# Performance work log

Measured on AMD Instinct MI355X. Metric: run time of the kernel, lower is better.

## Reference

```python
import jax, jax.numpy as jnp
import numpy as np

B, S, D, H, L, F = 16, 256, 512, 1024, 2, 2048  # batch, seq, inner, head(clusters), layers, ffnn
HID = D // 2
LN_EPS = 1e-5


def _lstm_dir(x, Wih, Whh, bih, bhh, reverse=False):
    # x: [B,S,D] -> hs: [B,S,HID]; PyTorch gate order i,f,g,o
    if reverse:
        x = x[:, ::-1]
    xT = jnp.swapaxes(x, 0, 1)                    # [S,B,D]
    pre = xT @ Wih.T + (bih + bhh)                # precompute input contribution [S,B,4*HID]
    z = jnp.zeros((x.shape[0], Whh.shape[1]), x.dtype)

    def step(carry, p):
        h, c = carry
        g = p + h @ Whh.T
        i, f, gg, o = jnp.split(g, 4, axis=-1)
        c = jax.nn.sigmoid(f) * c + jax.nn.sigmoid(i) * jnp.tanh(gg)
        h = jax.nn.sigmoid(o) * jnp.tanh(c)
        return (h, c), h

    _, hs = jax.lax.scan(step, (z, z), pre)
    hs = jnp.swapaxes(hs, 0, 1)                   # [B,S,HID]
    if reverse:
        hs = hs[:, ::-1]
    return hs


def _layernorm(x, g, b):
    mu = jnp.mean(x, axis=-1, keepdims=True)
    var = jnp.mean(jnp.square(x - mu), axis=-1, keepdims=True)
    return (x - mu) * jax.lax.rsqrt(var + LN_EPS) * g + b


def _forward(input_sequence, label_embeddings, out_proj,
             Wih_f, Whh_f, bih_f, bhh_f, Wih_b, Whh_b, bih_b, bhh_b,
             ffnn_w1, ffnn_b1, ffnn_w2, ffnn_b2, ln_g, ln_b):
    fwd = _lstm_dir(input_sequence, Wih_f, Whh_f, bih_f, bhh_f, reverse=False)
    bwd = _lstm_dir(input_sequence, Wih_b, Whh_b, bih_b, bhh_b, reverse=True)
    features = jnp.concatenate([fwd, bwd], axis=-1)          # [B,S,D]

    query = jnp.broadcast_to(label_embeddings, (input_sequence.shape[0], H, D))
    for l in range(L):
        # self-attention (no scaling, as in source)
        w = jax.nn.softmax(jnp.einsum('bqd,bkd->bqk', query, query), axis=-1)
        q1 = jnp.einsum('bqk,bkd->bqd', w, query)
        # cross-attention onto LSTM features
        w2 = jax.nn.softmax(jnp.einsum('bqd,bsd->bqs', q1, features), axis=-1)
        q2 = jnp.einsum('bqs,bsd->bqd', w2, features)
        # FFN + LayerNorm
        h = jax.nn.gelu(q2 @ ffnn_w1[l] + ffnn_b1[l], approximate=False) @ ffnn_w2[l] + ffnn_b2[l]
        query = _layernorm(h, ln_g[l], ln_b[l])
    # (query @ output) * eye @ ones  ==  diagonal of the matmul == batched dot
    return jnp.einsum('bhd,dh->bh', query, out_proj)


def setup_inputs() -> dict:
    ks = jax.random.split(jax.random.key(0), 20)
    s_lstm = 1.0 / np.sqrt(HID)
    s_ff = 0.02
    clusters = jax.random.normal(ks[0], (H, D), jnp.float32) * s_ff
    return {
        'input_sequence': jax.random.normal(ks[1], (B, S, D), jnp.float32),
        'label_embeddings': clusters,
        'out_proj': clusters.T,
        'Wih_f': jax.random.normal(ks[2], (4 * HID, D), jnp.float32) * s_lstm,
        'Whh_f': jax.random.normal(ks[3], (4 * HID, HID), jnp.float32) * s_lstm,
        'bih_f': jax.random.normal(ks[4], (4 * HID,), jnp.float32) * s_lstm,
        'bhh_f': jax.random.normal(ks[5], (4 * HID,), jnp.float32) * s_lstm,
        'Wih_b': jax.random.normal(ks[6], (4 * HID, D), jnp.float32) * s_lstm,
        'Whh_b': jax.random.normal(ks[7], (4 * HID, HID), jnp.float32) * s_lstm,
        'bih_b': jax.random.normal(ks[8], (4 * HID,), jnp.float32) * s_lstm,
        'bhh_b': jax.random.normal(ks[9], (4 * HID,), jnp.float32) * s_lstm,
        'ffnn_w1': jax.random.normal(ks[10], (L, D, F), jnp.float32) * s_ff,
        'ffnn_b1': jnp.zeros((L, F), jnp.float32),
        'ffnn_w2': jax.random.normal(ks[11], (L, F, D), jnp.float32) * s_ff,
        'ffnn_b2': jnp.zeros((L, D), jnp.float32),
        'ln_g': jnp.ones((L, D), jnp.float32),
        'ln_b': jnp.zeros((L, D), jnp.float32),
    }


def reference(input_sequence, label_embeddings, out_proj,
              Wih_f, Whh_f, bih_f, bhh_f, Wih_b, Whh_b, bih_b, bhh_b,
              ffnn_w1, ffnn_b1, ffnn_w2, ffnn_b2, ln_g, ln_b):
    return _forward(input_sequence, label_embeddings, out_proj,
                    Wih_f, Whh_f, bih_f, bhh_f, Wih_b, Whh_b, bih_b, bhh_b,
                    ffnn_w1, ffnn_b1, ffnn_w2, ffnn_b2, ln_g, ln_b)
```

## Files before the change

kernel.cpp:

```cpp
#include <hip/hip_runtime.h>
#include <hip/hip_bf16.h>
#include <math.h>

#define NB 16
#define NS 256
#define ND 512
#define NH 1024
#define NF 2048
#define NHID 256

typedef __attribute__((ext_vector_type(8))) short bf16x8;
typedef __attribute__((ext_vector_type(4))) float f32x4;

__device__ __forceinline__ unsigned short f2bf(float f) {
    unsigned u = __float_as_uint(f);
    unsigned r = u + 0x7fffu + ((u >> 16) & 1u);
    return (unsigned short)(r >> 16);
}
__device__ __forceinline__ float bf2f(unsigned short h) {
    return __uint_as_float(((unsigned)h) << 16);
}
__device__ __forceinline__ float sigmoid_fast(float x) {
    return 1.0f / (1.0f + __expf(-x));
}
__device__ __forceinline__ float tanh_fast(float x) {
    return 1.0f - 2.0f / (__expf(2.0f * x) + 1.0f);
}

template<int PASSES, int ACT, int OUT>
__global__ __launch_bounds__(256) void sgemm4(
    const unsigned short* __restrict__ Ahi, const unsigned short* __restrict__ Alo,
    const unsigned short* __restrict__ Bhi, const unsigned short* __restrict__ Blo,
    const float* __restrict__ bias,
    float* __restrict__ C, unsigned short* __restrict__ Chi, unsigned short* __restrict__ Clo,
    int M, int N, int K, int lda, int ldb, long sA, long sB, long sC)
{
    __shared__ unsigned short Ah[128 * 32];
    __shared__ unsigned short Bh[128 * 32];
    __shared__ unsigned short Al[(PASSES == 3) ? 128 * 32 : 64];
    __shared__ unsigned short Bl[(PASSES == 3) ? 128 * 32 : 64];

    const int t = threadIdx.x;
    const int z = blockIdx.z;
    const int m0 = blockIdx.y * 128, n0 = blockIdx.x * 128;
    const int wid = t >> 6, lane = t & 63;
    const int wr = (wid >> 1) * 64, wc = (wid & 1) * 64;
    const int lr = lane & 15, lk = lane >> 4;
    const int rl = lane >> 2, sl = lane & 3;

    const unsigned short* pAh = Ahi + (size_t)z * sA;
    const unsigned short* pBh = Bhi + (size_t)z * sB;
    const unsigned short* pAl = (PASSES == 3) ? Alo + (size_t)z * sA : nullptr;
    const unsigned short* pBl = (PASSES == 3) ? Blo + (size_t)z * sB : nullptr;

    f32x4 acc[4][4];
    #pragma unroll
    for (int i = 0; i < 4; ++i)
        #pragma unroll
        for (int j = 0; j < 4; ++j) acc[i][j] = (f32x4){0.f, 0.f, 0.f, 0.f};

    for (int k0 = 0; k0 < K; k0 += 32) {
        #pragma unroll
        for (int e = 0; e < 2; ++e) {
            const int r = e * 64 + wid * 16 + rl;
            const size_t goA = (size_t)(m0 + r) * lda + k0 + sl * 8;
            const size_t goB = (size_t)(n0 + r) * ldb + k0 + sl * 8;
            const int lo = (e * 64 + wid * 16) * 32;
            __builtin_amdgcn_global_load_lds((const void*)(pAh + goA), (void*)&Ah[lo], 16, 0, 0);
            __builtin_amdgcn_global_load_lds((const void*)(pBh + goB), (void*)&Bh[lo], 16, 0, 0);
            if (PASSES == 3) {
                __builtin_amdgcn_global_load_lds((const void*)(pAl + goA), (void*)&Al[lo], 16, 0, 0);
                __builtin_amdgcn_global_load_lds((const void*)(pBl + goB), (void*)&Bl[lo], 16, 0, 0);
            }
        }
        __syncthreads();

        bf16x8 ah[4], bh[4], al[4], bl[4];
        #pragma unroll
        for (int mt = 0; mt < 4; ++mt) {
            int rf = wr + mt * 16 + lr;
            ah[mt] = *(const bf16x8*)&Ah[rf * 32 + lk * 8];
            if (PASSES == 3) al[mt] = *(const bf16x8*)&Al[rf * 32 + lk * 8];
        }
        #pragma unroll
        for (int nt = 0; nt < 4; ++nt) {
            int rf = wc + nt * 16 + lr;
            bh[nt] = *(const bf16x8*)&Bh[rf * 32 + lk * 8];
            if (PASSES == 3) bl[nt] = *(const bf16x8*)&Bl[rf * 32 + lk * 8];
        }
        #pragma unroll
        for (int mt = 0; mt < 4; ++mt)
            #pragma unroll
            for (int nt = 0; nt < 4; ++nt) {
                acc[mt][nt] = __builtin_amdgcn_mfma_f32_16x16x32_bf16(ah[mt], bh[nt], acc[mt][nt], 0, 0, 0);
                if (PASSES == 3) {
                    acc[mt][nt] = __builtin_amdgcn_mfma_f32_16x16x32_bf16(al[mt], bh[nt], acc[mt][nt], 0, 0, 0);
                    acc[mt][nt] = __builtin_amdgcn_mfma_f32_16x16x32_bf16(ah[mt], bl[nt], acc[mt][nt], 0, 0, 0);
                }
            }
        __syncthreads();
    }

    #pragma unroll
    for (int nt = 0; nt < 4; ++nt) {
        int col = n0 + wc + nt * 16 + lr;
        float bv = bias ? bias[col] : 0.0f;
        #pragma unroll
        for (int mt = 0; mt < 4; ++mt) {
            #pragma unroll
            for (int i = 0; i < 4; ++i) {
                int row = m0 + wr + mt * 16 + lk * 4 + i;
                float x = acc[mt][nt][i] + bv;
                if (ACT == 1) x = 0.5f * x * (1.0f + erff(x * 0.70710678118654752f));
                size_t oi = (size_t)z * sC + (size_t)row * N + col;
                if (OUT == 1) {
                    unsigned short h = f2bf(x);
                    Chi[oi] = h;
                    Clo[oi] = f2bf(x - bf2f(h));
                } else if (OUT == 2) {
                    Chi[oi] = f2bf(x);
                } else {
                    C[oi] = x;
                }
            }
        }
    }
}

static void gemm4(int passes, int act, int outm,
                  const unsigned short* Ahi, const unsigned short* Alo,
                  const unsigned short* Bhi, const unsigned short* Blo,
                  const float* bias, float* C, unsigned short* Chi, unsigned short* Clo,
                  int M, int N, int K, int lda, int ldb,
                  long sA, long sB, long sC, int Z, hipStream_t st)
{
    dim3 g(N / 128, M / 128, Z), b(256);
    if (passes == 3) {
        sgemm4<3, 0, 0><<<g, b, 0, st>>>(Ahi, Alo, Bhi, Blo, bias, C, Chi, Clo, M, N, K, lda, ldb, sA, sB, sC);
    } else if (outm == 1) {
        sgemm4<1, 0, 1><<<g, b, 0, st>>>(Ahi, Alo, Bhi, Blo, bias, C, Chi, Clo, M, N, K, lda, ldb, sA, sB, sC);
    } else if (outm == 2 && act == 1) {
        sgemm4<1, 1, 2><<<g, b, 0, st>>>(Ahi, Alo, Bhi, Blo, bias, C, Chi, Clo, M, N, K, lda, ldb, sA, sB, sC);
    } else if (outm == 2) {
        sgemm4<1, 0, 2><<<g, b, 0, st>>>(Ahi, Alo, Bhi, Blo, bias, C, Chi, Clo, M, N, K, lda, ldb, sA, sB, sC);
    } else {
        sgemm4<1, 0, 0><<<g, b, 0, st>>>(Ahi, Alo, Bhi, Blo, bias, C, Chi, Clo, M, N, K, lda, ldb, sA, sB, sC);
    }
}

__global__ __launch_bounds__(256) void cvt_split(const float* __restrict__ in,
                                                 unsigned short* __restrict__ hi,
                                                 unsigned short* __restrict__ lo)
{
    size_t i = ((size_t)blockIdx.x * 256 + threadIdx.x) * 4;
    float4 v = *(const float4*)(in + i);
    ushort4 h, l;
    h.x = f2bf(v.x); l.x = f2bf(v.x - bf2f(h.x));
    h.y = f2bf(v.y); l.y = f2bf(v.y - bf2f(h.y));
    h.z = f2bf(v.z); l.z = f2bf(v.z - bf2f(h.z));
    h.w = f2bf(v.w); l.w = f2bf(v.w - bf2f(h.w));
    *(ushort4*)(hi + i) = h;
    *(ushort4*)(lo + i) = l;
}

__global__ __launch_bounds__(256) void cvt_split_t(const float* __restrict__ in,
                                                   unsigned short* __restrict__ hiT,
                                                   unsigned short* __restrict__ loT,
                                                   int R, int C)
{
    __shared__ unsigned short tileH[64 * 72];
    __shared__ unsigned short tileL[64 * 72];
    int r0 = blockIdx.y * 64, c0 = blockIdx.x * 64;
    int t = threadIdx.x;
    int tr = t >> 2, tc = (t & 3) * 16;

    float v[16];
    const float* src = in + (size_t)(r0 + tr) * C + c0 + tc;
    *(float4*)(v)      = *(const float4*)(src);
    *(float4*)(v + 4)  = *(const float4*)(src + 4);
    *(float4*)(v + 8)  = *(const float4*)(src + 8);
    *(float4*)(v + 12) = *(const float4*)(src + 12);
    #pragma unroll
    for (int i = 0; i < 16; ++i) {
        unsigned short h = f2bf(v[i]);
        tileH[(tc + i) * 72 + tr] = h;
        tileL[(tc + i) * 72 + tr] = f2bf(v[i] - bf2f(h));
    }
    __syncthreads();

    size_t ob = (size_t)(c0 + tr) * R + r0 + tc;
    *(uint4*)(hiT + ob)     = *(const uint4*)(&tileH[tr * 72 + tc]);
    *(uint4*)(hiT + ob + 8) = *(const uint4*)(&tileH[tr * 72 + tc + 8]);
    *(uint4*)(loT + ob)     = *(const uint4*)(&tileL[tr * 72 + tc]);
    *(uint4*)(loT + ob + 8) = *(const uint4*)(&tileL[tr * 72 + tc + 8]);
}

__global__ __launch_bounds__(256) void tcvt_bf16(const unsigned short* __restrict__ in,
                                                 unsigned short* __restrict__ out,
                                                 int R, int C)
{
    __shared__ unsigned short tile[64 * 72];
    int z = blockIdx.z;
    in += (size_t)z * R * C;
    out += (size_t)z * R * C;
    int r0 = blockIdx.y * 64, c0 = blockIdx.x * 64;
    int t = threadIdx.x;
    int tr = t >> 2, tc = (t & 3) * 16;

    uint4 q0 = *(const uint4*)(in + (size_t)(r0 + tr) * C + c0 + tc);
    uint4 q1 = *(const uint4*)(in + (size_t)(r0 + tr) * C + c0 + tc + 8);
    unsigned short e[16];
    *(uint4*)(e) = q0;
    *(uint4*)(e + 8) = q1;
    #pragma unroll
    for (int i = 0; i < 16; ++i) tile[(tc + i) * 72 + tr] = e[i];
    __syncthreads();

    uint4 o0 = *(const uint4*)(&tile[tr * 72 + tc]);
    uint4 o1 = *(const uint4*)(&tile[tr * 72 + tc + 8]);
    *(uint4*)(out + (size_t)(c0 + tr) * R + r0 + tc) = o0;
    *(uint4*)(out + (size_t)(c0 + tr) * R + r0 + tc + 8) = o1;
}

__global__ __launch_bounds__(256) void bias_sum_kernel(
    const float* bihF, const float* bhhF, const float* bihB, const float* bhhB,
    float* out)
{
    int i = blockIdx.x * 256 + threadIdx.x;
    if (i < 1024) out[i] = bihF[i] + bhhF[i];
    else out[i] = bihB[i - 1024] + bhhB[i - 1024];
}

__global__ __launch_bounds__(256) void rec_fused(
    const float* __restrict__ pre,
    const float* __restrict__ WhhF, const float* __restrict__ WhhB,
    unsigned long long* __restrict__ hg, int* __restrict__ flags,
    unsigned short* __restrict__ fhi, unsigned short* __restrict__ flo,
    const unsigned short* __restrict__ lehi, const unsigned short* __restrict__ lelo,
    float* __restrict__ wsc,
    const float* __restrict__ w1, const float* __restrict__ w2,
    unsigned short* __restrict__ w1th0, unsigned short* __restrict__ w2th0,
    unsigned short* __restrict__ w1th1, unsigned short* __restrict__ w2th1,
    const float* __restrict__ proj,
    unsigned short* __restrict__ pth, unsigned short* __restrict__ ptl)
{
    __shared__ unsigned short hh[16 * 264];
    __shared__ unsigned short hl[16 * 264];
    __shared__ float gx[4][16][17];
    __shared__ unsigned short gAh[128 * 32];
    __shared__ unsigned short gAl[128 * 32];
    __shared__ unsigned short gBh[128 * 32];
    __shared__ unsigned short gBl[128 * 32];
    __shared__ unsigned short tH[64 * 72];
    __shared__ unsigned short tL[64 * 72];

    const int tid = threadIdx.x;

    if (blockIdx.x < 32) {
        const int bid = blockIdx.x;
        const int dir = bid >> 4, slice = bid & 15;
        const float* Whh = dir ? WhhB : WhhF;
        const int wv = tid >> 6;
        const int lane = tid & 63;
        const int lr = lane & 15;
        const int lk = lane >> 4;
        const int eb = tid >> 4;
        const int eu = tid & 15;

        bf16x8 wfh[8], wfl[8];
        {
            const float* wrow = Whh + (size_t)(wv * 256 + slice * 16 + lr) * 256 + lk * 8;
            #pragma unroll
            for (int kt = 0; kt < 8; ++kt) {
                float4 a = *(const float4*)(wrow + kt * 32);
                float4 b = *(const float4*)(wrow + kt * 32 + 4);
                float v[8] = {a.x, a.y, a.z, a.w, b.x, b.y, b.z, b.w};
                unsigned short hhv[8], llv[8];
                #pragma unroll
                for (int i = 0; i < 8; ++i) {
                    unsigned short h = f2bf(v[i]);
                    hhv[i] = h;
                    llv[i] = f2bf(v[i] - bf2f(h));
                }
                wfh[kt] = *(bf16x8*)hhv;
                wfl[kt] = *(bf16x8*)llv;
            }
        }
        for (int i = tid; i < 16 * 264; i += 256) { hh[i] = 0; hl[i] = 0; }

        float c = 0.0f;
        __syncthreads();

        for (int si = 0; si < NS; ++si) {
            const int s = dir ? (NS - 1 - si) : si;
            const float* pp = pre + ((size_t)(eb * NS + s)) * 2048 + dir * 1024 + slice * 16 + eu;
            float pi = pp[0], pf = pp[256], pg = pp[512], po = pp[768];

            if (si > 0) {
                if (tid < 16) {
                    while (__hip_atomic_load(&flags[dir * 16 + tid], __ATOMIC_RELAXED,
                                             __HIP_MEMORY_SCOPE_AGENT) < si) {
                        __builtin_amdgcn_s_sleep(1);
                    }
                }
                __syncthreads();
                const unsigned long long* src =
                    hg + (size_t)(((si - 1) & 1) * 2 + dir) * 2048;
                const int b2 = tid >> 4, pb = (tid & 15) * 8;
                unsigned short hbuf[16], lbuf[16];
                #pragma unroll
                for (int j = 0; j < 8; ++j) {
                    unsigned long long v = __hip_atomic_load(
                        &src[b2 * 128 + pb + j], __ATOMIC_RELAXED,
                        __HIP_MEMORY_SCOPE_AGENT);
                    hbuf[2 * j]     = (unsigned short)(v & 0xffff);
                    lbuf[2 * j]     = (unsigned short)((v >> 16) & 0xffff);
                    hbuf[2 * j + 1] = (unsigned short)((v >> 32) & 0xffff);
                    lbuf[2 * j + 1] = (unsigned short)(v >> 48);
                }
                char* dh = (char*)hh + b2 * 528 + (tid & 15) * 32;
                char* dl = (char*)hl + b2 * 528 + (tid & 15) * 32;
                *(uint4*)dh        = *(uint4*)(hbuf);
                *(uint4*)(dh + 16) = *(uint4*)(hbuf + 8);
                *(uint4*)dl        = *(uint4*)(lbuf);
                *(uint4*)(dl + 16) = *(uint4*)(lbuf + 8);
                __syncthreads();
            }

            f32x4 acc = (f32x4){0.f, 0.f, 0.f, 0.f};
            #pragma unroll
            for (int kt = 0; kt < 8; ++kt) {
                const char* hp = (const char*)hh + lr * 528 + kt * 64 + lk * 16;
                const char* lp = (const char*)hl + lr * 528 + kt * 64 + lk * 16;
                bf16x8 ah = *(const bf16x8*)hp;
                bf16x8 al = *(const bf16x8*)lp;
                acc = __builtin_amdgcn_mfma_f32_16x16x32_bf16(ah, wfh[kt], acc, 0, 0, 0);
                acc = __builtin_amdgcn_mfma_f32_16x16x32_bf16(al, wfh[kt], acc, 0, 0, 0);
                acc = __builtin_amdgcn_mfma_f32_16x16x32_bf16(ah, wfl[kt], acc, 0, 0, 0);
            }
            #pragma unroll
            for (int i = 0; i < 4; ++i) gx[wv][lk * 4 + i][lr] = acc[i];
            __syncthreads();

            float ai = gx[0][eb][eu] + pi;
            float af = gx[1][eb][eu] + pf;
            float ag = gx[2][eb][eu] + pg;
            float ao = gx[3][eb][eu] + po;
            float gi = sigmoid_fast(ai);
            float gf = sigmoid_fast(af);
            float gg = tanh_fast(ag);
            float go = sigmoid_fast(ao);
            c = gf * c + gi * gg;
            float h = go * tanh_fast(c);

            unsigned short h16 = f2bf(h);
            unsigned short l16 = f2bf(h - bf2f(h16));
            unsigned my = (unsigned)h16 | ((unsigned)l16 << 16);
            unsigned oth = __shfl_xor(my, 1);
            if ((eu & 1) == 0) {
                unsigned long long v = (unsigned long long)my |
                                       ((unsigned long long)oth << 32);
                unsigned long long* dst =
                    hg + (size_t)((si & 1) * 2 + dir) * 2048;
                __hip_atomic_store(&dst[eb * 128 + slice * 8 + (eu >> 1)], v,
                                   __ATOMIC_RELAXED, __HIP_MEMORY_SCOPE_AGENT);
            }
            size_t oi = ((size_t)(eb * NS + s)) * 512 + dir * 256 + slice * 16 + eu;
            fhi[oi] = h16;
            flo[oi] = l16;

            asm volatile("s_waitcnt vmcnt(0)" ::: "memory");
            __syncthreads();
            if (tid == 0)
                __hip_atomic_store(&flags[bid], si + 1, __ATOMIC_RELAXED,
                                   __HIP_MEMORY_SCOPE_AGENT);
        }
        return;
    }

    const int hid = blockIdx.x - 32;
    const int lane = tid & 63;
    const int wid = tid >> 6;
    const int lr = lane & 15, lk = lane >> 4;

    if (hid < 64) {
        const int m0 = (hid >> 3) * 128, n0 = (hid & 7) * 128;
        const int wr = (wid >> 1) * 64, wc = (wid & 1) * 64;
        const int sr = tid >> 1, sc = (tid & 1) * 16;

        f32x4 acc[4][4];
        #pragma unroll
        for (int i = 0; i < 4; ++i)
            #pragma unroll
            for (int j = 0; j < 4; ++j) acc[i][j] = (f32x4){0.f, 0.f, 0.f, 0.f};

        for (int k0 = 0; k0 < ND; k0 += 32) {
            {
                size_t oa = (size_t)(m0 + sr) * ND + k0 + sc;
                size_t ob = (size_t)(n0 + sr) * ND + k0 + sc;
                *(uint4*)&gAh[sr * 32 + sc]     = *(const uint4*)(lehi + oa);
                *(uint4*)&gAh[sr * 32 + sc + 8] = *(const uint4*)(lehi + oa + 8);
                *(uint4*)&gAl[sr * 32 + sc]     = *(const uint4*)(lelo + oa);
                *(uint4*)&gAl[sr * 32 + sc + 8] = *(const uint4*)(lelo + oa + 8);
                *(uint4*)&gBh[sr * 32 + sc]     = *(const uint4*)(lehi + ob);
                *(uint4*)&gBh[sr * 32 + sc + 8] = *(const uint4*)(lehi + ob + 8);
                *(uint4*)&gBl[sr * 32 + sc]     = *(const uint4*)(lelo + ob);
                *(uint4*)&gBl[sr * 32 + sc + 8] = *(const uint4*)(lelo + ob + 8);
            }
            __syncthreads();

            bf16x8 ah[4], al[4], bh[4], bl[4];
            #pragma unroll
            for (int mt = 0; mt < 4; ++mt) {
                int rf = wr + mt * 16 + lr;
                ah[mt] = *(const bf16x8*)&gAh[rf * 32 + lk * 8];
                al[mt] = *(const bf16x8*)&gAl[rf * 32 + lk * 8];
            }
            #pragma unroll
            for (int nt = 0; nt < 4; ++nt) {
                int rf = wc + nt * 16 + lr;
                bh[nt] = *(const bf16x8*)&gBh[rf * 32 + lk * 8];
                bl[nt] = *(const bf16x8*)&gBl[rf * 32 + lk * 8];
            }
            #pragma unroll
            for (int mt = 0; mt < 4; ++mt)
                #pragma unroll
                for (int nt = 0; nt < 4; ++nt) {
                    acc[mt][nt] = __builtin_amdgcn_mfma_f32_16x16x32_bf16(ah[mt], bh[nt], acc[mt][nt], 0, 0, 0);
                    acc[mt][nt] = __builtin_amdgcn_mfma_f32_16x16x32_bf16(al[mt], bh[nt], acc[mt][nt], 0, 0, 0);
                    acc[mt][nt] = __builtin_amdgcn_mfma_f32_16x16x32_bf16(ah[mt], bl[nt], acc[mt][nt], 0, 0, 0);
                }
            __syncthreads();
        }
        const int wr2 = (wid >> 1) * 64, wc2 = (wid & 1) * 64;
        #pragma unroll
        for (int nt = 0; nt < 4; ++nt) {
            int col = n0 + wc2 + nt * 16 + lr;
            #pragma unroll
            for (int mt = 0; mt < 4; ++mt)
                #pragma unroll
                for (int i = 0; i < 4; ++i) {
                    int row = m0 + wr2 + mt * 16 + lk * 4 + i;
                    wsc[(size_t)row * NH + col] = acc[mt][nt][i];
                }
        }
    }

    const int tr = tid >> 2, tc = (tid & 3) * 16;
    for (int job = hid; job < 1152; job += 224) {
        const float* in;
        unsigned short* outH;
        unsigned short* outL = nullptr;
        int R, C, by, bx;
        if (job < 256)        { int j = job;        in = w1;              outH = w1th0; R = ND; C = NF; by = j >> 5, bx = j & 31; }
        else if (job < 512)   { int j = job - 256;  in = w2;              outH = w2th0; R = NF; C = ND; by = j >> 3, bx = j & 7; }
        else if (job < 768)   { int j = job - 512;  in = w1 + (size_t)ND * NF; outH = w1th1; R = ND; C = NF; by = j >> 5, bx = j & 31; }
        else if (job < 1024)  { int j = job - 768;  in = w2 + (size_t)NF * ND; outH = w2th1; R = NF; C = ND; by = j >> 3, bx = j & 7; }
        else                  { int j = job - 1024; in = proj;            outH = pth; outL = ptl; R = 512; C = 1024; by = j >> 4, bx = j & 15; }

        int r0 = by * 64, c0 = bx * 64;
        __syncthreads();
        float v[16];
        const float* src = in + (size_t)(r0 + tr) * C + c0 + tc;
        *(float4*)(v)      = *(const float4*)(src);
        *(float4*)(v + 4)  = *(const float4*)(src + 4);
        *(float4*)(v + 8)  = *(const float4*)(src + 8);
        *(float4*)(v + 12) = *(const float4*)(src + 12);
        if (outL) {
            #pragma unroll
            for (int i = 0; i < 16; ++i) {
                unsigned short h = f2bf(v[i]);
                tH[(tc + i) * 72 + tr] = h;
                tL[(tc + i) * 72 + tr] = f2bf(v[i] - bf2f(h));
            }
        } else {
            #pragma unroll
            for (int i = 0; i < 16; ++i) tH[(tc + i) * 72 + tr] = f2bf(v[i]);
        }
        __syncthreads();
        size_t ob = (size_t)(c0 + tr) * R + r0 + tc;
        *(uint4*)(outH + ob)     = *(const uint4*)(&tH[tr * 72 + tc]);
        *(uint4*)(outH + ob + 8) = *(const uint4*)(&tH[tr * 72 + tc + 8]);
        if (outL) {
            *(uint4*)(outL + ob)     = *(const uint4*)(&tL[tr * 72 + tc]);
            *(uint4*)(outL + ob + 8) = *(const uint4*)(&tL[tr * 72 + tc + 8]);
        }
    }
}

__global__ __launch_bounds__(256) void softmax_ip(float* __restrict__ X, int N)
{
    float* row = X + (size_t)blockIdx.x * N;
    unsigned short* o = (unsigned short*)row;
    int t = threadIdx.x;
    int cnt = N >> 8;
    float v[4];
    float m = -1e30f;
    for (int i = 0; i < cnt; ++i) { v[i] = row[t + (i << 8)]; m = fmaxf(m, v[i]); }
    for (int sh = 32; sh; sh >>= 1) m = fmaxf(m, __shfl_xor(m, sh));
    __shared__ float lm[4];
    if ((t & 63) == 0) lm[t >> 6] = m;
    __syncthreads();
    m = fmaxf(fmaxf(lm[0], lm[1]), fmaxf(lm[2], lm[3]));
    float s = 0.0f;
    for (int i = 0; i < cnt; ++i) { v[i] = expf(v[i] - m); s += v[i]; }
    for (int sh = 32; sh; sh >>= 1) s += __shfl_xor(s, sh);
    __shared__ float ls[4];
    if ((t & 63) == 0) ls[t >> 6] = s;
    __syncthreads();
    s = ls[0] + ls[1] + ls[2] + ls[3];
    float inv = 1.0f / s;
    __syncthreads();
    for (int i = 0; i < cnt; ++i) {
        float y = v[i] * inv;
        unsigned short h = f2bf(y);
        int j = t + (i << 8);
        o[j] = h;
        o[N + j] = f2bf(y - bf2f(h));
    }
}

__global__ __launch_bounds__(256) void layernorm_split(
    const float* __restrict__ X, const float* __restrict__ g, const float* __restrict__ b,
    unsigned short* __restrict__ ohi, unsigned short* __restrict__ olo)
{
    const float* row = X + (size_t)blockIdx.x * 512;
    size_t ob = (size_t)blockIdx.x * 512;
    int t = threadIdx.x;
    float x0 = row[t], x1 = row[t + 256];
    float s = x0 + x1, sq = x0 * x0 + x1 * x1;
    for (int o = 32; o; o >>= 1) { s += __shfl_xor(s, o); sq += __shfl_xor(sq, o); }
    __shared__ float ls[8];
    int w = t >> 6;
    if ((t & 63) == 0) { ls[w] = s; ls[4 + w] = sq; }
    __syncthreads();
    s = ls[0] + ls[1] + ls[2] + ls[3];
    sq = ls[4] + ls[5] + ls[6] + ls[7];
    float mu = s * (1.0f / 512.0f);
    float var = sq * (1.0f / 512.0f) - mu * mu;
    float inv = rsqrtf(var + 1e-5f);
    float y0 = (x0 - mu) * inv * g[t]       + b[t];
    float y1 = (x1 - mu) * inv * g[t + 256] + b[t + 256];
    unsigned short h0 = f2bf(y0), h1 = f2bf(y1);
    ohi[ob + t]       = h0;  olo[ob + t]       = f2bf(y0 - bf2f(h0));
    ohi[ob + t + 256] = h1;  olo[ob + t + 256] = f2bf(y1 - bf2f(h1));
}

__global__ __launch_bounds__(256) void outproj3(
    const unsigned short* __restrict__ qhi, const unsigned short* __restrict__ qlo,
    const unsigned short* __restrict__ phi, const unsigned short* __restrict__ plo,
    float* __restrict__ out)
{
    int gw = blockIdx.x * 4 + (threadIdx.x >> 6);
    int lane = threadIdx.x & 63;
    int h = gw & 1023;
    uint4 qh = ((const uint4*)(qhi + (size_t)gw * 512))[lane];
    uint4 ql = ((const uint4*)(qlo + (size_t)gw * 512))[lane];
    uint4 ph = ((const uint4*)(phi + (size_t)h * 512))[lane];
    uint4 pl = ((const uint4*)(plo + (size_t)h * 512))[lane];
    unsigned short qhe[8], qle[8], phe[8], ple[8];
    *(uint4*)qhe = qh; *(uint4*)qle = ql; *(uint4*)phe = ph; *(uint4*)ple = pl;
    float s = 0.0f;
    #pragma unroll
    for (int i = 0; i < 8; ++i) {
        float q = bf2f(qhe[i]) + bf2f(qle[i]);
        float p = bf2f(phe[i]) + bf2f(ple[i]);
        s += q * p;
    }
    for (int o = 32; o; o >>= 1) s += __shfl_xor(s, o);
    if (lane == 0) out[gw] = s;
}

extern "C" void kernel_launch(void* const* d_in, const int* in_sizes, int n_in,
                              void* d_out, int out_size, void* d_ws, size_t ws_size,
                              hipStream_t stream)
{
    (void)in_sizes; (void)n_in; (void)out_size; (void)ws_size;

    const float* x     = (const float*)d_in[0];
    const float* le    = (const float*)d_in[1];
    const float* proj  = (const float*)d_in[2];
    const float* WihF  = (const float*)d_in[3];
    const float* WhhF  = (const float*)d_in[4];
    const float* bihF  = (const float*)d_in[5];
    const float* bhhF  = (const float*)d_in[6];
    const float* WihB  = (const float*)d_in[7];
    const float* WhhB  = (const float*)d_in[8];
    const float* bihB  = (const float*)d_in[9];
    const float* bhhB  = (const float*)d_in[10];
    const float* w1    = (const float*)d_in[11];
    const float* b1    = (const float*)d_in[12];
    const float* w2    = (const float*)d_in[13];
    const float* b2    = (const float*)d_in[14];
    const float* lng   = (const float*)d_in[15];
    const float* lnb   = (const float*)d_in[16];
    float* out = (float*)d_out;
    float* ws  = (float*)d_ws;
    unsigned short* wsu = (unsigned short*)d_ws;

    const size_t MEG = 1048576;
    const size_t R0    = 0;
    const size_t R1    = 8 * MEG;
    const size_t AR    = 16 * MEG;
    const size_t QHI   = 33 * MEG;
    const size_t QLO   = 37 * MEG;
    const size_t FHI   = 41 * MEG;
    const size_t FLO   = 42 * MEG;
    const size_t FTHI  = 43 * MEG;
    const size_t FTLO  = 44 * MEG;
    const size_t LEHI  = 45 * MEG;
    const size_t LELO  = LEHI  + MEG / 4;
    const size_t LETHI = LELO  + MEG / 4;
    const size_t LETLO = LETHI + MEG / 4;
    const size_t WIHH  = 46 * MEG;
    const size_t WIHL  = WIHH + MEG / 2;
    const size_t SYNC  = 47 * MEG;
    const size_t W1TH0 = SYNC  + MEG / 4;
    const size_t W1TH1 = W1TH0 + MEG / 2;
    const size_t W2TH0 = W1TH1 + MEG / 2;
    const size_t W2TH1 = W2TH0 + MEG / 2;
    const size_t PTH   = W2TH1 + MEG / 2;
    const size_t PTL   = PTH   + MEG / 4;
    const size_t BSUM  = PTL   + MEG / 4;

    float* pre    = ws + R0;
    float* lnsrc  = ws + R0;
    float* arena  = ws + AR;
    float* bsum   = ws + BSUM;
    int*   flags  = (int*)(ws + SYNC);
    unsigned long long* hg = (unsigned long long*)(ws + SYNC + 1024);
    unsigned short* qthi  = wsu + 2 * R0;
    unsigned short* q2hi  = wsu + 2 * R1;
    unsigned short* qhi   = wsu + 2 * QHI;
    unsigned short* qlo   = wsu + 2 * QLO;
    unsigned short* fhi   = wsu + 2 * FHI;
    unsigned short* flo   = wsu + 2 * FLO;
    unsigned short* fthi  = wsu + 2 * FTHI;
    unsigned short* ftlo  = wsu + 2 * FTLO;
    unsigned short* lehi  = wsu + 2 * LEHI;
    unsigned short* lelo  = wsu + 2 * LELO;
    unsigned short* lethi = wsu + 2 * LETHI;
    unsigned short* letlo = wsu + 2 * LETLO;
    unsigned short* wihh  = wsu + 2 * WIHH;
    unsigned short* wihl  = wsu + 2 * WIHL;
    unsigned short* w1th0 = wsu + 2 * W1TH0;
    unsigned short* w1th1 = wsu + 2 * W1TH1;
    unsigned short* w2th0 = wsu + 2 * W2TH0;
    unsigned short* w2th1 = wsu + 2 * W2TH1;
    unsigned short* pth   = wsu + 2 * PTH;
    unsigned short* ptl   = wsu + 2 * PTL;

    bias_sum_kernel<<<8, 256, 0, stream>>>(bihF, bhhF, bihB, bhhB, bsum);
    cvt_split<<<512, 256, 0, stream>>>(WihF, wihh, wihl);
    cvt_split<<<512, 256, 0, stream>>>(WihB, wihh + 524288, wihl + 524288);
    cvt_split<<<512, 256, 0, stream>>>(le, lehi, lelo);
    { dim3 g(512 / 64, 1024 / 64, 1);
      cvt_split_t<<<g, 256, 0, stream>>>(le, lethi, letlo, 1024, 512); }
    hipMemsetAsync(flags, 0, 32 * sizeof(int), stream);

    unsigned short* xhi = wsu + 2 * AR;
    unsigned short* xlo = wsu + 2 * (AR + MEG);
    cvt_split<<<2048, 256, 0, stream>>>(x, xhi, xlo);

    gemm4(3, 0, 0, xhi, xlo, wihh, wihl, bsum, pre, nullptr, nullptr,
          NB * NS, 2048, ND, ND, ND, 0, 0, 0, 1, stream);

    float* wsc_l0 = arena;
    rec_fused<<<256, 256, 0, stream>>>(pre, WhhF, WhhB, hg, flags, fhi, flo,
                                       lehi, lelo, wsc_l0,
                                       w1, w2, w1th0, w2th0, w1th1, w2th1,
                                       proj, pth, ptl);
    { dim3 g(512 / 64, 256 / 64, 16);
      tcvt_bf16<<<g, 256, 0, stream>>>(fhi, fthi, 256, 512);
      tcvt_bf16<<<g, 256, 0, stream>>>(flo, ftlo, 256, 512); }

    for (int l = 0; l < 2; ++l) {
        const float* b1l = b1 + (size_t)l * NF;
        const float* b2l = b2 + (size_t)l * ND;
        const float* gl  = lng + (size_t)l * ND;
        const float* bl  = lnb + (size_t)l * ND;
        unsigned short* w1th = l ? w1th1 : w1th0;
        unsigned short* w2th = l ? w2th1 : w2th0;

        if (l == 0) {
            float* wsc = wsc_l0;
            unsigned short* wscu = (unsigned short*)wsc;
            unsigned short* q1hi = wsu + 2 * (AR + 1 * MEG);
            unsigned short* q1lo = wsu + 2 * (AR + 1 * MEG + MEG / 4);
            float* s2s = arena + 4 * MEG;
            unsigned short* s2u = (unsigned short*)s2s;

            softmax_ip<<<NH, 256, 0, stream>>>(wsc, NH);
            gemm4(1, 0, 1, wscu, nullptr, lethi, nullptr, nullptr, nullptr, q1hi, q1lo,
                  NH, ND, NH, 2 * NH, NH, 0, 0, 0, 1, stream);
            gemm4(3, 0, 0, q1hi, q1lo, fhi, flo, nullptr, s2s, nullptr, nullptr,
                  NH, NS, ND, ND, ND, 0, (long)NS * ND, (long)NH * NS, 16, stream);
            softmax_ip<<<NB * NH, 256, 0, stream>>>(s2s, NS);
            gemm4(1, 0, 2, s2u, nullptr, fthi, nullptr, nullptr, nullptr, q2hi, nullptr,
                  NH, ND, NS, 2 * NS, NS,
                  (long)2 * NH * NS, (long)ND * NS, (long)NH * ND, 16, stream);
        } else {
            { dim3 g(512 / 64, 1024 / 64, 16);
              tcvt_bf16<<<g, 256, 0, stream>>>(qhi, qthi, 1024, 512); }
            float* wsc = arena;
            unsigned short* wscu = (unsigned short*)wsc;
            unsigned short* q1hi = wsu + 2 * (AR + 8 * MEG);
            unsigned short* q1lo = wsu + 2 * (AR + 10 * MEG);
            float* s2s = arena + 12 * MEG;
            unsigned short* s2u = (unsigned short*)s2s;
            for (int g8 = 0; g8 < 2; ++g8) {
                size_t qo = (size_t)g8 * 8;
                gemm4(3, 0, 0, qhi + qo * NH * ND, qlo + qo * NH * ND,
                      qhi + qo * NH * ND, qlo + qo * NH * ND, nullptr, wsc, nullptr, nullptr,
                      NH, NH, ND, ND, ND,
                      (long)NH * ND, (long)NH * ND, (long)NH * NH, 8, stream);
                softmax_ip<<<8 * NH, 256, 0, stream>>>(wsc, NH);
                gemm4(1, 0, 1, wscu, nullptr, qthi + qo * ND * NH, nullptr,
                      nullptr, nullptr, q1hi, q1lo, NH, ND, NH, 2 * NH, NH,
                      (long)2 * NH * NH, (long)ND * NH, (long)NH * ND, 8, stream);
                gemm4(3, 0, 0, q1hi, q1lo, fhi + qo * NS * ND, flo + qo * NS * ND,
                      nullptr, s2s, nullptr, nullptr, NH, NS, ND, ND, ND,
                      (long)NH * ND, (long)NS * ND, (long)NH * NS, 8, stream);
                softmax_ip<<<8 * NH, 256, 0, stream>>>(s2s, NS);
                gemm4(1, 0, 2, s2u, nullptr, fthi + qo * ND * NS, nullptr,
                      nullptr, nullptr, q2hi + qo * NH * ND, nullptr,
                      NH, ND, NS, 2 * NS, NS,
                      (long)2 * NH * NS, (long)ND * NS, (long)NH * ND, 8, stream);
            }
        }

        unsigned short* ffhi = wsu + 2 * AR;
        gemm4(1, 1, 2, q2hi, nullptr, w1th, nullptr, b1l, nullptr, ffhi, nullptr,
              16384, NF, ND, ND, ND, 0, 0, 0, 1, stream);
        gemm4(1, 0, 0, ffhi, nullptr, w2th, nullptr, b2l, lnsrc, nullptr, nullptr,
              16384, ND, NF, NF, NF, 0, 0, 0, 1, stream);
        layernorm_split<<<NB * NH, 256, 0, stream>>>(lnsrc, gl, bl, qhi, qlo);
    }

    outproj3<<<4096, 256, 0, stream>>>(qhi, qlo, pth, ptl, out);
}
```

Before: 1.510 ms.

## Fuse FFN second GEMM with LayerNorm and merge post-recurrence transposes with softmax

Adds an ffn2_ln kernel in which each block computes a 64x512 full-row output tile of the second FFN GEMM, then applies bias and LayerNorm in registers and writes the bf16 hi/lo split directly. This removes the fp32 intermediate round trip and the separate layernorm launch. It also merges the two feature transposes and the layer-0 self-attention softmax into one post_rec launch. The cost is that the fused GEMM launches only 256 blocks with a simple single-buffered K loop, which may use the GPU less efficiently than the tuned 128x128 GEMM.

New measurement: 1.502 ms. About the same (-0.5%).

```diff
diff --git a/kernel.cpp b/kernel.cpp
--- a/kernel.cpp
+++ b/kernel.cpp
@@ -146,6 +146,124 @@
     } else {
         sgemm4<1, 0, 0><<<g, b, 0, st>>>(Ahi, Alo, Bhi, Blo, bias, C, Chi, Clo, M, N, K, lda, ldb, sA, sB, sC);
     }
+}
+
+__global__ __launch_bounds__(256) void ffn2_ln(
+    const unsigned short* __restrict__ A, const unsigned short* __restrict__ B,
+    const float* __restrict__ bias, const float* __restrict__ g, const float* __restrict__ bb,
+    unsigned short* __restrict__ Ohi, unsigned short* __restrict__ Olo)
+{
+    __shared__ unsigned short Ah[64 * 32];
+    __shared__ unsigned short Bh[512 * 32];
+    __shared__ float stats[64][4][2];
+
+    const int t = threadIdx.x;
+    const int m0 = blockIdx.x * 64;
+    const int wid = t >> 6, lane = t & 63;
+    const int lr = lane & 15, lk = lane >> 4;
+    const int wc = wid * 128;
+    const int rl = lane >> 2, sl = lane & 3;
+
+    f32x4 acc[4][8];
+    #pragma unroll
+    for (int i = 0; i < 4; ++i)
+        #pragma unroll
+        for (int j = 0; j < 8; ++j) acc[i][j] = (f32x4){0.f, 0.f, 0.f, 0.f};
+
+    for (int k0 = 0; k0 < NF; k0 += 32) {
+        __builtin_amdgcn_global_load_lds(
+            (const void*)(A + (size_t)(m0 + wid * 16 + rl) * NF + k0 + sl * 8),
+            (void*)&Ah[(wid * 16) * 32], 16, 0, 0);
+        #pragma unroll
+        for (int e = 0; e < 8; ++e) {
+            int r = e * 64 + wid * 16 + rl;
+            __builtin_amdgcn_global_load_lds(
+                (const void*)(B + (size_t)r * NF + k0 + sl * 8),
+                (void*)&Bh[(e * 64 + wid * 16) * 32], 16, 0, 0);
+        }
+        __syncthreads();
+
+        bf16x8 af[4], bf[8];
+        #pragma unroll
+        for (int mt = 0; mt < 4; ++mt)
+            af[mt] = *(const bf16x8*)&Ah[(mt * 16 + lr) * 32 + lk * 8];
+        #pragma unroll
+        for (int nt = 0; nt < 8; ++nt)
+            bf[nt] = *(const bf16x8*)&Bh[(wc + nt * 16 + lr) * 32 + lk * 8];
+        #pragma unroll
+        for (int mt = 0; mt < 4; ++mt)
+            #pragma unroll
+            for (int nt = 0; nt < 8; ++nt)
+                acc[mt][nt] = __builtin_amdgcn_mfma_f32_16x16x32_bf16(af[mt], bf[nt], acc[mt][nt], 0, 0, 0);
+        __syncthreads();
+    }
+
+    float bv[8];
+    #pragma unroll
+    for (int nt = 0; nt < 8; ++nt) bv[nt] = bias[wc + nt * 16 + lr];
+
+    float psum[4][4], psq[4][4];
+    #pragma unroll
+    for (int mt = 0; mt < 4; ++mt)
+        #pragma unroll
+        for (int i = 0; i < 4; ++i) {
+            float s = 0.f, q = 0.f;
+            #pragma unroll
+            for (int nt = 0; nt < 8; ++nt) {
+                float x = acc[mt][nt][i] + bv[nt];
+                acc[mt][nt][i] = x;
+                s += x;
+                q += x * x;
+            }
+            psum[mt][i] = s;
+            psq[mt][i] = q;
+        }
+    #pragma unroll
+    for (int o = 1; o <= 8; o <<= 1)
+        #pragma unroll
+        for (int mt = 0; mt < 4; ++mt)
+            #pragma unroll
+            for (int i = 0; i < 4; ++i) {
+                psum[mt][i] += __shfl_xor(psum[mt][i], o);
+                psq[mt][i]  += __shfl_xor(psq[mt][i], o);
+            }
+    if (lr == 0) {
+        #pragma unroll
+        for (int mt = 0; mt < 4; ++mt)
+            #pragma unroll
+            for (int i = 0; i < 4; ++i) {
+                int r = mt * 16 + lk * 4 + i;
+                stats[r][wid][0] = psum[mt][i];
+                stats[r][wid][1] = psq[mt][i];
+            }
+    }
+    __syncthreads();
+
+    float gv[8], betav[8];
+    #pragma unroll
+    for (int nt = 0; nt < 8; ++nt) {
+        gv[nt]    = g[wc + nt * 16 + lr];
+        betav[nt] = bb[wc + nt * 16 + lr];
+    }
+    #pragma unroll
+    for (int mt = 0; mt < 4; ++mt)
+        #pragma unroll
+        for (int i = 0; i < 4; ++i) {
+            int r = mt * 16 + lk * 4 + i;
+            float s = stats[r][0][0] + stats[r][1][0] + stats[r][2][0] + stats[r][3][0];
+            float q = stats[r][0][1] + stats[r][1][1] + stats[r][2][1] + stats[r][3][1];
+            float mu = s * (1.0f / 512.0f);
+            float var = q * (1.0f / 512.0f) - mu * mu;
+            float inv = rsqrtf(var + 1e-5f);
+            #pragma unroll
+            for (int nt = 0; nt < 8; ++nt) {
+                float y = (acc[mt][nt][i] - mu) * inv * gv[nt] + betav[nt];
+                size_t oi = (size_t)(m0 + r) * 512 + wc + nt * 16 + lr;
+                unsigned short h = f2bf(y);
+                Ohi[oi] = h;
+                Olo[oi] = f2bf(y - bf2f(h));
+            }
+        }
 }
 
 __global__ __launch_bounds__(256) void cvt_split(const float* __restrict__ in,
@@ -488,6 +606,73 @@
     }
 }
 
+__global__ __launch_bounds__(256) void post_rec(
+    const unsigned short* __restrict__ fhi, const unsigned short* __restrict__ flo,
+    unsigned short* __restrict__ fthi, unsigned short* __restrict__ ftlo,
+    float* __restrict__ wsc)
+{
+    __shared__ unsigned short tile[64 * 72];
+    __shared__ float lm[4];
+    __shared__ float ls[4];
+    const int t = threadIdx.x;
+
+    if (blockIdx.x < 1024) {
+        int job = blockIdx.x;
+        const unsigned short* in;
+        unsigned short* out;
+        if (job < 512) { in = fhi; out = fthi; } else { in = flo; out = ftlo; job -= 512; }
+        const int R = 256, C = 512;
+        int z = job >> 5, jj = job & 31;
+        int bx = jj & 7, by = jj >> 3;
+        in  += (size_t)z * R * C;
+        out += (size_t)z * R * C;
+        int r0 = by * 64, c0 = bx * 64;
+        int tr = t >> 2, tc = (t & 3) * 16;
+
+        uint4 q0 = *(const uint4*)(in + (size_t)(r0 + tr) * C + c0 + tc);
+        uint4 q1 = *(const uint4*)(in + (size_t)(r0 + tr) * C + c0 + tc + 8);
+        unsigned short e[16];
+        *(uint4*)(e) = q0;
+        *(uint4*)(e + 8) = q1;
+        #pragma unroll
+        for (int i = 0; i < 16; ++i) tile[(tc + i) * 72 + tr] = e[i];
+        __syncthreads();
+
+        *(uint4*)(out + (size_t)(c0 + tr) * R + r0 + tc)     = *(const uint4*)(&tile[tr * 72 + tc]);
+        *(uint4*)(out + (size_t)(c0 + tr) * R + r0 + tc + 8) = *(const uint4*)(&tile[tr * 72 + tc + 8]);
+        return;
+    }
+
+    const int N = 1024;
+    float* row = wsc + (size_t)(blockIdx.x - 1024) * N;
+    unsigned short* o = (unsigned short*)row;
+    float v[4];
+    float m = -1e30f;
+    #pragma unroll
+    for (int i = 0; i < 4; ++i) { v[i] = row[t + (i << 8)]; m = fmaxf(m, v[i]); }
+    for (int sh = 32; sh; sh >>= 1) m = fmaxf(m, __shfl_xor(m, sh));
+    if ((t & 63) == 0) lm[t >> 6] = m;
+    __syncthreads();
+    m = fmaxf(fmaxf(lm[0], lm[1]), fmaxf(lm[2], lm[3]));
+    float s = 0.0f;
+    #pragma unroll
+    for (int i = 0; i < 4; ++i) { v[i] = expf(v[i] - m); s += v[i]; }
+    for (int sh = 32; sh; sh >>= 1) s += __shfl_xor(s, sh);
+    if ((t & 63) == 0) ls[t >> 6] = s;
+    __syncthreads();
+    s = ls[0] + ls[1] + ls[2] + ls[3];
+    float inv = 1.0f / s;
+    __syncthreads();
+    #pragma unroll
+    for (int i = 0; i < 4; ++i) {
+        float y = v[i] * inv;
+        unsigned short h = f2bf(y);
+        int j = t + (i << 8);
+        o[j] = h;
+        o[N + j] = f2bf(y - bf2f(h));
+    }
+}
+
 __global__ __launch_bounds__(256) void softmax_ip(float* __restrict__ X, int N)
 {
     float* row = X + (size_t)blockIdx.x * N;
@@ -520,32 +705,6 @@
     }
 }
 
-__global__ __launch_bounds__(256) void layernorm_split(
-    const float* __restrict__ X, const float* __restrict__ g, const float* __restrict__ b,
-    unsigned short* __restrict__ ohi, unsigned short* __restrict__ olo)
-{
-    const float* row = X + (size_t)blockIdx.x * 512;
-    size_t ob = (size_t)blockIdx.x * 512;
-    int t = threadIdx.x;
-    float x0 = row[t], x1 = row[t + 256];
-    float s = x0 + x1, sq = x0 * x0 + x1 * x1;
-    for (int o = 32; o; o >>= 1) { s += __shfl_xor(s, o); sq += __shfl_xor(sq, o); }
-    __shared__ float ls[8];
-    int w = t >> 6;
-    if ((t & 63) == 0) { ls[w] = s; ls[4 + w] = sq; }
-    __syncthreads();
-    s = ls[0] + ls[1] + ls[2] + ls[3];
-    sq = ls[4] + ls[5] + ls[6] + ls[7];
-    float mu = s * (1.0f / 512.0f);
-    float var = sq * (1.0f / 512.0f) - mu * mu;
-    float inv = rsqrtf(var + 1e-5f);
-    float y0 = (x0 - mu) * inv * g[t]       + b[t];
-    float y1 = (x1 - mu) * inv * g[t + 256] + b[t + 256];
-    unsigned short h0 = f2bf(y0), h1 = f2bf(y1);
-    ohi[ob + t]       = h0;  olo[ob + t]       = f2bf(y0 - bf2f(h0));
-    ohi[ob + t + 256] = h1;  olo[ob + t + 256] = f2bf(y1 - bf2f(h1));
-}
-
 __global__ __launch_bounds__(256) void outproj3(
     const unsigned short* __restrict__ qhi, const unsigned short* __restrict__ qlo,
     const unsigned short* __restrict__ phi, const unsigned short* __restrict__ plo,
@@ -624,7 +783,6 @@
     const size_t BSUM  = PTL   + MEG / 4;
 
     float* pre    = ws + R0;
-    float* lnsrc  = ws + R0;
     float* arena  = ws + AR;
     float* bsum   = ws + BSUM;
     int*   flags  = (int*)(ws + SYNC);
@@ -670,9 +828,8 @@
                                        lehi, lelo, wsc_l0,
                                        w1, w2, w1th0, w2th0, w1th1, w2th1,
                                        proj, pth, ptl);
-    { dim3 g(512 / 64, 256 / 64, 16);
-      tcvt_bf16<<<g, 256, 0, stream>>>(fhi, fthi, 256, 512);
-      tcvt_bf16<<<g, 256, 0, stream>>>(flo, ftlo, 256, 512); }
+
+    post_rec<<<2048, 256, 0, stream>>>(fhi, flo, fthi, ftlo, wsc_l0);
 
     for (int l = 0; l < 2; ++l) {
         const float* b1l = b1 + (size_t)l * NF;
@@ -683,14 +840,12 @@
         unsigned short* w2th = l ? w2th1 : w2th0;
 
         if (l == 0) {
-            float* wsc = wsc_l0;
-            unsigned short* wscu = (unsigned short*)wsc;
+            unsigned short* wscu = (unsigned short*)wsc_l0;
             unsigned short* q1hi = wsu + 2 * (AR + 1 * MEG);
             unsigned short* q1lo = wsu + 2 * (AR + 1 * MEG + MEG / 4);
             float* s2s = arena + 4 * MEG;
             unsigned short* s2u = (unsigned short*)s2s;
 
-            softmax_ip<<<NH, 256, 0, stream>>>(wsc, NH);
             gemm4(1, 0, 1, wscu, nullptr, lethi, nullptr, nullptr, nullptr, q1hi, q1lo,
                   NH, ND, NH, 2 * NH, NH, 0, 0, 0, 1, stream);
             gemm4(3, 0, 0, q1hi, q1lo, fhi, flo, nullptr, s2s, nullptr, nullptr,
@@ -732,9 +887,7 @@
         unsigned short* ffhi = wsu + 2 * AR;
         gemm4(1, 1, 2, q2hi, nullptr, w1th, nullptr, b1l, nullptr, ffhi, nullptr,
               16384, NF, ND, ND, ND, 0, 0, 0, 1, stream);
-        gemm4(1, 0, 0, ffhi, nullptr, w2th, nullptr, b2l, lnsrc, nullptr, nullptr,
-              16384, ND, NF, NF, NF, 0, 0, 0, 1, stream);
-        layernorm_split<<<NB * NH, 256, 0, stream>>>(lnsrc, gl, bl, qhi, qlo);
+        ffn2_ln<<<256, 256, 0, stream>>>(ffhi, w2th, b2l, gl, bl, qhi, qlo);
     }
 
     outproj3<<<4096, 256, 0, stream>>>(qhi, qlo, pth, ptl, out);
```
